# Performance work log

Measured on AMD Instinct MI355X. Metric: run time of the kernel, lower is better.

Reference implementation:

```python
import jax, jax.numpy as jnp
import numpy as np

WH, WW = 7, 7          # window size
SH, SW = 3, 3          # shift size
NUM_HEADS = 8


def setup_inputs() -> dict:
    key = jax.random.key(0)
    ks = jax.random.split(key, 5)
    B, H, W, C = 32, 56, 56, 256
    return {
        "x": jax.random.normal(ks[0], (B, H * W, C), dtype=jnp.float32),
        "w_qkv": jax.random.normal(ks[1], (C, 3 * C), dtype=jnp.float32) * (C ** -0.5),
        "b_qkv": jax.random.normal(ks[2], (3 * C,), dtype=jnp.float32) * 0.02,
        "w_proj": jax.random.normal(ks[3], (C, C), dtype=jnp.float32) * (C ** -0.5),
        "b_proj": jax.random.normal(ks[4], (C,), dtype=jnp.float32) * 0.02,
        "H": H,
        "W": W,
    }


def reference(x, w_qkv, b_qkv, w_proj, b_proj, H, W):
    B, N, C = x.shape
    nh = NUM_HEADS
    hd = C // nh
    nwh, nww = H // WH, W // WW

    xi = x.reshape(B, H, W, C)
    if SH > 0 or SW > 0:
        xi = jnp.roll(xi, shift=(-SH, -SW), axis=(1, 2))
    # window partition: [B*nwh*nww, WH*WW, C]
    xw = xi.reshape(B, nwh, WH, nww, WW, C).transpose(0, 1, 3, 2, 4, 5)
    xw = xw.reshape(-1, WH * WW, C)

    qkv = xw @ w_qkv + b_qkv                     # [nW, 49, 3C]
    qkv = qkv.reshape(-1, WH * WW, 3, nh, hd).transpose(2, 0, 3, 1, 4)
    q, k, v = qkv[0], qkv[1], qkv[2]             # each [nW, nh, 49, hd]

    attn = jnp.einsum('whqd,whkd->whqk', q, k) * (hd ** -0.5)
    attn = jax.nn.softmax(attn, axis=-1)
    out = jnp.einsum('whqk,whkd->whqd', attn, v)  # [nW, nh, 49, hd]
    out = out.transpose(0, 2, 1, 3).reshape(-1, WH * WW, C)
    out = out @ w_proj + b_proj

    # window merge
    out = out.reshape(B, nwh, nww, WH, WW, C).transpose(0, 1, 3, 2, 4, 5)
    out = out.reshape(B, H, W, C)
    if SH > 0 or SW > 0:
        out = jnp.roll(out, shift=(SH, SW), axis=(1, 2))
    return out.reshape(B, N, C)
```

## Files before the change

### kernel.cpp

```cpp
#include <hip/hip_runtime.h>
#include <hip/hip_bf16.h>

typedef __attribute__((ext_vector_type(4))) short bf16x4;
typedef __attribute__((ext_vector_type(8))) short bf16x8;
typedef __attribute__((ext_vector_type(4))) float f32x4;

#define MFMA32(A,B,C) __builtin_amdgcn_mfma_f32_16x16x32_bf16(A,B,C,0,0,0)
#define ROWB 528
#define ROWS 49

__device__ __forceinline__ short f2bf(float f) {
    __hip_bfloat16 h = __float2bfloat16(f);
    union { __hip_bfloat16 h; short s; } u; u.h = h;
    return u.s;
}

__global__ void prep_weights(const float* __restrict__ wqkv,
                             const float* __restrict__ wproj,
                             short* __restrict__ wqkvT,
                             short* __restrict__ wprojT) {
    const int n = blockIdx.x, k = threadIdx.x;
    if (n < 768) wqkvT[n * 256 + k] = f2bf(wqkv[k * 768 + n]);
    else         wprojT[(n - 768) * 256 + k] = f2bf(wproj[k * 256 + (n - 768)]);
}

__launch_bounds__(256, 2)
__global__ void winattn_fused(const float* __restrict__ x,
                              const float* __restrict__ bqkv,
                              const float* __restrict__ bproj,
                              const short* __restrict__ wqkvT,
                              const short* __restrict__ wprojT,
                              float* __restrict__ out) {
    __shared__ char smem[2 * ROWS * ROWB];
    char* cbuf = smem + ROWS * ROWB;
    const int tid = threadIdx.x;
    const int wid = blockIdx.x;
    const int b  = wid >> 6;
    const int wh = (wid >> 3) & 7;
    const int ww = wid & 7;

    {
        const int r   = tid >> 2;
        const int qtr = tid & 3;
        if (r < ROWS) {
            char* dst = smem + r * ROWB + qtr * 128;
            const int i = r / 7, j = r - i * 7;
            int h  = wh * 7 + i + 3; if (h  >= 56) h  -= 56;
            int wc = ww * 7 + j + 3; if (wc >= 56) wc -= 56;
            const float* src = x + (((size_t)(b * 56 + h)) * 56 + wc) * 256 + qtr * 64;
            #pragma unroll
            for (int c = 0; c < 8; ++c) {
                f32x4 f0 = *(const f32x4*)(src + c * 8);
                f32x4 f1 = *(const f32x4*)(src + c * 8 + 4);
                bf16x8 o;
                #pragma unroll
                for (int q = 0; q < 4; ++q) { o[q] = f2bf(f0[q]); o[q + 4] = f2bf(f1[q]); }
                *(bf16x8*)(dst + c * 16) = o;
            }
        }
    }
    __syncthreads();

    const int wv4 = tid >> 6;
    const int l   = tid & 63;
    const int l15 = l & 15;
    const int l4  = l >> 4;

    const char* xb[4];
    #pragma unroll
    for (int t = 0; t < 4; ++t) {
        int row = t * 16 + l15; if (row > 48) row = 48;
        xb[t] = smem + row * ROWB + (l4 << 4);
    }
    const int rowoff = l15 * 256 + (l4 << 3);

    #pragma unroll
    for (int hh = 0; hh < 2; ++hh) {
        const int head = (hh << 2) + wv4;
        const short* wqB = wqkvT + ((head << 5) << 8);
        const short* wkB = wqB + (256 << 8);
        const short* wvB = wqB + (512 << 8);

        bf16x8 qp[4], kp[4], vp[2][2];

        #pragma unroll
        for (int h = 0; h < 2; ++h) {
            f32x4 acc[4];
            #pragma unroll
            for (int t = 0; t < 4; ++t) acc[t] = (f32x4){0.f, 0.f, 0.f, 0.f};
            const short* wp = wqB + (h << 12) + rowoff;
            #pragma unroll
            for (int kk = 0; kk < 8; ++kk) {
                bf16x8 wf = *(const bf16x8*)(wp + (kk << 5));
                #pragma unroll
                for (int t = 0; t < 4; ++t) {
                    bf16x8 xf = *(const bf16x8*)(xb[t] + kk * 64);
                    acc[t] = MFMA32(wf, xf, acc[t]);
                }
            }
            f32x4 bq = *(const f32x4*)(bqkv + (head << 5) + h * 16 + (l4 << 2));
            #pragma unroll
            for (int t = 0; t < 4; ++t)
                #pragma unroll
                for (int rg = 0; rg < 4; ++rg)
                    qp[t][h * 4 + rg] = f2bf((acc[t][rg] + bq[rg]) * 0.17677669529663687f);
        }
        #pragma unroll
        for (int h = 0; h < 2; ++h) {
            f32x4 acc[4];
            #pragma unroll
            for (int t = 0; t < 4; ++t) acc[t] = (f32x4){0.f, 0.f, 0.f, 0.f};
            const short* wp = wkB + (h << 12) + rowoff;
            #pragma unroll
            for (int kk = 0; kk < 8; ++kk) {
                bf16x8 wf = *(const bf16x8*)(wp + (kk << 5));
                #pragma unroll
                for (int t = 0; t < 4; ++t) {
                    bf16x8 xf = *(const bf16x8*)(xb[t] + kk * 64);
                    acc[t] = MFMA32(wf, xf, acc[t]);
                }
            }
            f32x4 bk = *(const f32x4*)(bqkv + 256 + (head << 5) + h * 16 + (l4 << 2));
            #pragma unroll
            for (int t = 0; t < 4; ++t)
                #pragma unroll
                for (int rg = 0; rg < 4; ++rg)
                    kp[t][h * 4 + rg] = f2bf(acc[t][rg] + bk[rg]);
        }
        #pragma unroll
        for (int h = 0; h < 2; ++h) {
            f32x4 acc[4];
            #pragma unroll
            for (int t = 0; t < 4; ++t) acc[t] = (f32x4){0.f, 0.f, 0.f, 0.f};
            const short* wp = wvB + (h << 12) + rowoff;
            #pragma unroll
            for (int kk = 0; kk < 8; ++kk) {
                bf16x8 wf = *(const bf16x8*)(wp + (kk << 5));
                #pragma unroll
                for (int t = 0; t < 4; ++t) {
                    bf16x8 xf = *(const bf16x8*)(xb[t] + kk * 64);
                    acc[t] = MFMA32(xf, wf, acc[t]);
                }
            }
            const float bv = bqkv[512 + (head << 5) + h * 16 + l15];
            #pragma unroll
            for (int t = 0; t < 4; ++t)
                #pragma unroll
                for (int rg = 0; rg < 4; ++rg)
                    vp[t >> 1][h][(t & 1) * 4 + rg] = f2bf(acc[t][rg] + bv);
        }

        #pragma unroll
        for (int qt = 0; qt < 4; ++qt) {
            f32x4 sQ[4];
            #pragma unroll
            for (int t = 0; t < 4; ++t) sQ[t] = (f32x4){0.f, 0.f, 0.f, 0.f};
            #pragma unroll
            for (int t = 0; t < 4; ++t)
                sQ[t] = MFMA32(kp[t], qp[qt], sQ[t]);

            float m = -1e30f;
            #pragma unroll
            for (int t = 0; t < 4; ++t)
                #pragma unroll
                for (int rg = 0; rg < 4; ++rg) {
                    const bool valid = (t < 3) || ((l4 | rg) == 0);
                    float v0 = valid ? sQ[t][rg] : -1e30f;
                    sQ[t][rg] = v0;
                    m = fmaxf(m, v0);
                }
            m = fmaxf(m, __shfl_xor(m, 16));
            m = fmaxf(m, __shfl_xor(m, 32));
            float s = 0.f;
            #pragma unroll
            for (int t = 0; t < 4; ++t)
                #pragma unroll
                for (int rg = 0; rg < 4; ++rg) {
                    float e = __expf(sQ[t][rg] - m);
                    sQ[t][rg] = e;
                    s += e;
                }
            s += __shfl_xor(s, 16);
            s += __shfl_xor(s, 32);
            const float inv = 1.f / s;

            bf16x8 pf[2];
            #pragma unroll
            for (int t = 0; t < 4; ++t)
                #pragma unroll
                for (int rg = 0; rg < 4; ++rg)
                    pf[t >> 1][(t & 1) * 4 + rg] = f2bf(sQ[t][rg] * inv);

            const int row = qt * 16 + l15;
            #pragma unroll
            for (int h = 0; h < 2; ++h) {
                f32x4 oq = (f32x4){0.f, 0.f, 0.f, 0.f};
                oq = MFMA32(vp[0][h], pf[0], oq);
                oq = MFMA32(vp[1][h], pf[1], oq);
                if (row < ROWS) {
                    bf16x4 ob;
                    #pragma unroll
                    for (int rg = 0; rg < 4; ++rg) ob[rg] = f2bf(oq[rg]);
                    const int colbyte = ((head << 5) + (h << 4) + (l4 << 2)) * 2;
                    *(bf16x4*)(cbuf + row * ROWB + colbyte) = ob;
                }
            }
        }
    }
    __syncthreads();

    const char* ab[4];
    #pragma unroll
    for (int rt = 0; rt < 4; ++rt) {
        int row = rt * 16 + l15; if (row > 48) row = 48;
        ab[rt] = cbuf + row * ROWB + (l4 << 4);
    }
    const int hb = wh * 7 + 3;
    const int wb = ww * 7 + 3;

    #pragma unroll
    for (int g = 0; g < 2; ++g) {
        const int colbase = (wv4 << 6) + (g << 5);
        f32x4 po[2][4];
        #pragma unroll
        for (int c = 0; c < 2; ++c)
            #pragma unroll
            for (int r = 0; r < 4; ++r) po[c][r] = (f32x4){0.f, 0.f, 0.f, 0.f};

        const short* pb[2];
        #pragma unroll
        for (int ct = 0; ct < 2; ++ct)
            pb[ct] = wprojT + ((colbase + (ct << 4) + l15) << 8) + (l4 << 3);

        #pragma unroll
        for (int kk = 0; kk < 8; ++kk) {
            bf16x8 a[4];
            #pragma unroll
            for (int rt = 0; rt < 4; ++rt) a[rt] = *(const bf16x8*)(ab[rt] + kk * 64);
            #pragma unroll
            for (int ct = 0; ct < 2; ++ct) {
                bf16x8 bfr = *(const bf16x8*)(pb[ct] + (kk << 5));
                #pragma unroll
                for (int rt = 0; rt < 4; ++rt)
                    po[ct][rt] = MFMA32(a[rt], bfr, po[ct][rt]);
            }
        }

        #pragma unroll
        for (int ct = 0; ct < 2; ++ct) {
            const int col = colbase + (ct << 4) + l15;
            const float bias = bproj[col];
            #pragma unroll
            for (int rt = 0; rt < 4; ++rt) {
                const int r0 = rt * 16 + (l4 << 2);
                int i = r0 / 7;
                int j = r0 - i * 7;
                #pragma unroll
                for (int rg = 0; rg < 4; ++rg) {
                    const int row = r0 + rg;
                    if (row < 49) {
                        int h  = hb + i; if (h  >= 56) h  -= 56;
                        int wc = wb + j; if (wc >= 56) wc -= 56;
                        out[(((size_t)(b * 56 + h)) * 56 + wc) * 256 + col] = po[ct][rt][rg] + bias;
                    }
                    ++j; if (j == 7) { j = 0; ++i; }
                }
            }
        }
    }
}

extern "C" void kernel_launch(void* const* d_in, const int* in_sizes, int n_in,
                              void* d_out, int out_size, void* d_ws, size_t ws_size,
                              hipStream_t stream) {
    const float* x     = (const float*)d_in[0];
    const float* wqkv  = (const float*)d_in[1];
    const float* bqkv  = (const float*)d_in[2];
    const float* wproj = (const float*)d_in[3];
    const float* bproj = (const float*)d_in[4];
    float* out = (float*)d_out;

    short* wqkvT  = (short*)d_ws;
    short* wprojT = wqkvT + 768 * 256;

    prep_weights<<<dim3(1024), dim3(256), 0, stream>>>(wqkv, wproj, wqkvT, wprojT);
    winattn_fused<<<dim3(2048), dim3(256), 0, stream>>>(x, bqkv, bproj, wqkvT, wprojT, out);
}
```

Baseline: 153.1 us.

## Reuse single LDS buffer for attention output by staging head-0 result in registers

Shrinks shared memory from two 49-row buffers to one. The first head's attention output is held in registers until both heads' QKV projections have read x from LDS. After a barrier, the context output overwrites the x buffer. The softmax normalization also moves after the PV matmul, scaling the 16 outputs per row instead of the probabilities. Halving LDS per block could allow more resident blocks, at the cost of extra registers for the staged outputs, which may push register pressure against the 2-block launch bound.

After: 176.9 us. 1.16x slower.

```diff
diff --git a/kernel.cpp b/kernel.cpp
--- a/kernel.cpp
+++ b/kernel.cpp
@@ -24,6 +24,114 @@
     else         wprojT[(n - 768) * 256 + k] = f2bf(wproj[k * 256 + (n - 768)]);
 }
 
+__device__ __forceinline__ void qkv_pass(const short* __restrict__ wqB,
+                                         const float* __restrict__ bqkv, int head,
+                                         const char* const xb[4],
+                                         int rowoff, int l4, int l15,
+                                         bf16x8 qp[4], bf16x8 kp[4], bf16x8 vp[2][2]) {
+    #pragma unroll
+    for (int h = 0; h < 2; ++h) {
+        f32x4 acc[4];
+        #pragma unroll
+        for (int t = 0; t < 4; ++t) acc[t] = (f32x4){0.f, 0.f, 0.f, 0.f};
+        const short* wp = wqB + (h << 12) + rowoff;
+        #pragma unroll
+        for (int kk = 0; kk < 8; ++kk) {
+            bf16x8 wf = *(const bf16x8*)(wp + (kk << 5));
+            #pragma unroll
+            for (int t = 0; t < 4; ++t) {
+                bf16x8 xf = *(const bf16x8*)(xb[t] + kk * 64);
+                acc[t] = MFMA32(wf, xf, acc[t]);
+            }
+        }
+        f32x4 bq = *(const f32x4*)(bqkv + (head << 5) + h * 16 + (l4 << 2));
+        #pragma unroll
+        for (int t = 0; t < 4; ++t)
+            #pragma unroll
+            for (int rg = 0; rg < 4; ++rg)
+                qp[t][h * 4 + rg] = f2bf((acc[t][rg] + bq[rg]) * 0.17677669529663687f);
+    }
+    #pragma unroll
+    for (int h = 0; h < 2; ++h) {
+        f32x4 acc[4];
+        #pragma unroll
+        for (int t = 0; t < 4; ++t) acc[t] = (f32x4){0.f, 0.f, 0.f, 0.f};
+        const short* wp = wqB + (256 << 8) + (h << 12) + rowoff;
+        #pragma unroll
+        for (int kk = 0; kk < 8; ++kk) {
+            bf16x8 wf = *(const bf16x8*)(wp + (kk << 5));
+            #pragma unroll
+            for (int t = 0; t < 4; ++t) {
+                bf16x8 xf = *(const bf16x8*)(xb[t] + kk * 64);
+                acc[t] = MFMA32(wf, xf, acc[t]);
+            }
+        }
+        f32x4 bk = *(const f32x4*)(bqkv + 256 + (head << 5) + h * 16 + (l4 << 2));
+        #pragma unroll
+        for (int t = 0; t < 4; ++t)
+            #pragma unroll
+            for (int rg = 0; rg < 4; ++rg)
+                kp[t][h * 4 + rg] = f2bf(acc[t][rg] + bk[rg]);
+    }
+    #pragma unroll
+    for (int h = 0; h < 2; ++h) {
+        f32x4 acc[4];
+        #pragma unroll
+        for (int t = 0; t < 4; ++t) acc[t] = (f32x4){0.f, 0.f, 0.f, 0.f};
+        const short* wp = wqB + (512 << 8) + (h << 12) + rowoff;
+        #pragma unroll
+        for (int kk = 0; kk < 8; ++kk) {
+            bf16x8 wf = *(const bf16x8*)(wp + (kk << 5));
+            #pragma unroll
+            for (int t = 0; t < 4; ++t) {
+                bf16x8 xf = *(const bf16x8*)(xb[t] + kk * 64);
+                acc[t] = MFMA32(xf, wf, acc[t]);
+            }
+        }
+        const float bv = bqkv[512 + (head << 5) + h * 16 + l15];
+        #pragma unroll
+        for (int t = 0; t < 4; ++t)
+            #pragma unroll
+            for (int rg = 0; rg < 4; ++rg)
+                vp[t >> 1][h][(t & 1) * 4 + rg] = f2bf(acc[t][rg] + bv);
+    }
+}
+
+__device__ __forceinline__ float attn_pf(const bf16x8 kp[4], bf16x8 qpqt, int l4,
+                                         bf16x8 pf[2]) {
+    f32x4 sQ[4];
+    #pragma unroll
+    for (int t = 0; t < 4; ++t) sQ[t] = (f32x4){0.f, 0.f, 0.f, 0.f};
+    #pragma unroll
+    for (int t = 0; t < 4; ++t)
+        sQ[t] = MFMA32(kp[t], qpqt, sQ[t]);
+
+    float m = -1e30f;
+    #pragma unroll
+    for (int t = 0; t < 4; ++t)
+        #pragma unroll
+        for (int rg = 0; rg < 4; ++rg) {
+            const bool valid = (t < 3) || ((l4 | rg) == 0);
+            float v0 = valid ? sQ[t][rg] : -1e30f;
+            sQ[t][rg] = v0;
+            m = fmaxf(m, v0);
+        }
+    m = fmaxf(m, __shfl_xor(m, 16));
+    m = fmaxf(m, __shfl_xor(m, 32));
+    float s = 0.f;
+    #pragma unroll
+    for (int t = 0; t < 4; ++t)
+        #pragma unroll
+        for (int rg = 0; rg < 4; ++rg) {
+            float e = __expf(sQ[t][rg] - m);
+            pf[t >> 1][(t & 1) * 4 + rg] = f2bf(e);
+            s += e;
+        }
+    s += __shfl_xor(s, 16);
+    s += __shfl_xor(s, 32);
+    return 1.f / s;
+}
+
 __launch_bounds__(256, 2)
 __global__ void winattn_fused(const float* __restrict__ x,
                               const float* __restrict__ bqkv,
@@ -31,8 +139,7 @@
                               const short* __restrict__ wqkvT,
                               const short* __restrict__ wprojT,
                               float* __restrict__ out) {
-    __shared__ char smem[2 * ROWS * ROWB];
-    char* cbuf = smem + ROWS * ROWB;
+    __shared__ char smem[ROWS * ROWB];
     const int tid = threadIdx.x;
     const int wid = blockIdx.x;
     const int b  = wid >> 6;
@@ -74,136 +181,59 @@
     }
     const int rowoff = l15 * 256 + (l4 << 3);
 
-    #pragma unroll
-    for (int hh = 0; hh < 2; ++hh) {
-        const int head = (hh << 2) + wv4;
-        const short* wqB = wqkvT + ((head << 5) << 8);
-        const short* wkB = wqB + (256 << 8);
-        const short* wvB = wqB + (512 << 8);
-
-        bf16x8 qp[4], kp[4], vp[2][2];
-
-        #pragma unroll
-        for (int h = 0; h < 2; ++h) {
-            f32x4 acc[4];
-            #pragma unroll
-            for (int t = 0; t < 4; ++t) acc[t] = (f32x4){0.f, 0.f, 0.f, 0.f};
-            const short* wp = wqB + (h << 12) + rowoff;
-            #pragma unroll
-            for (int kk = 0; kk < 8; ++kk) {
-                bf16x8 wf = *(const bf16x8*)(wp + (kk << 5));
-                #pragma unroll
-                for (int t = 0; t < 4; ++t) {
-                    bf16x8 xf = *(const bf16x8*)(xb[t] + kk * 64);
-                    acc[t] = MFMA32(wf, xf, acc[t]);
-                }
-            }
-            f32x4 bq = *(const f32x4*)(bqkv + (head << 5) + h * 16 + (l4 << 2));
-            #pragma unroll
-            for (int t = 0; t < 4; ++t)
-                #pragma unroll
-                for (int rg = 0; rg < 4; ++rg)
-                    qp[t][h * 4 + rg] = f2bf((acc[t][rg] + bq[rg]) * 0.17677669529663687f);
-        }
-        #pragma unroll
-        for (int h = 0; h < 2; ++h) {
-            f32x4 acc[4];
-            #pragma unroll
-            for (int t = 0; t < 4; ++t) acc[t] = (f32x4){0.f, 0.f, 0.f, 0.f};
-            const short* wp = wkB + (h << 12) + rowoff;
-            #pragma unroll
-            for (int kk = 0; kk < 8; ++kk) {
-                bf16x8 wf = *(const bf16x8*)(wp + (kk << 5));
-                #pragma unroll
-                for (int t = 0; t < 4; ++t) {
-                    bf16x8 xf = *(const bf16x8*)(xb[t] + kk * 64);
-                    acc[t] = MFMA32(wf, xf, acc[t]);
-                }
-            }
-            f32x4 bk = *(const f32x4*)(bqkv + 256 + (head << 5) + h * 16 + (l4 << 2));
-            #pragma unroll
-            for (int t = 0; t < 4; ++t)
-                #pragma unroll
-                for (int rg = 0; rg < 4; ++rg)
-                    kp[t][h * 4 + rg] = f2bf(acc[t][rg] + bk[rg]);
-        }
-        #pragma unroll
-        for (int h = 0; h < 2; ++h) {
-            f32x4 acc[4];
-            #pragma unroll
-            for (int t = 0; t < 4; ++t) acc[t] = (f32x4){0.f, 0.f, 0.f, 0.f};
-            const short* wp = wvB + (h << 12) + rowoff;
-            #pragma unroll
-            for (int kk = 0; kk < 8; ++kk) {
-                bf16x8 wf = *(const bf16x8*)(wp + (kk << 5));
-                #pragma unroll
-                for (int t = 0; t < 4; ++t) {
-                    bf16x8 xf = *(const bf16x8*)(xb[t] + kk * 64);
-                    acc[t] = MFMA32(xf, wf, acc[t]);
-                }
-            }
-            const float bv = bqkv[512 + (head << 5) + h * 16 + l15];
-            #pragma unroll
-            for (int t = 0; t < 4; ++t)
-                #pragma unroll
-                for (int rg = 0; rg < 4; ++rg)
-                    vp[t >> 1][h][(t & 1) * 4 + rg] = f2bf(acc[t][rg] + bv);
-        }
-
+    bf16x8 qp[4], kp[4], vp[2][2];
+    bf16x4 oreg0[4][2];
+
+    {
+        const int head = wv4;
+        qkv_pass(wqkvT + ((head << 5) << 8), bqkv, head, xb, rowoff, l4, l15, qp, kp, vp);
         #pragma unroll
         for (int qt = 0; qt < 4; ++qt) {
-            f32x4 sQ[4];
-            #pragma unroll
-            for (int t = 0; t < 4; ++t) sQ[t] = (f32x4){0.f, 0.f, 0.f, 0.f};
-            #pragma unroll
-            for (int t = 0; t < 4; ++t)
-                sQ[t] = MFMA32(kp[t], qp[qt], sQ[t]);
-
-            float m = -1e30f;
-            #pragma unroll
-            for (int t = 0; t < 4; ++t)
-                #pragma unroll
-                for (int rg = 0; rg < 4; ++rg) {
-                    const bool valid = (t < 3) || ((l4 | rg) == 0);
-                    float v0 = valid ? sQ[t][rg] : -1e30f;
-                    sQ[t][rg] = v0;
-                    m = fmaxf(m, v0);
-                }
-            m = fmaxf(m, __shfl_xor(m, 16));
-            m = fmaxf(m, __shfl_xor(m, 32));
-            float s = 0.f;
-            #pragma unroll
-            for (int t = 0; t < 4; ++t)
-                #pragma unroll
-                for (int rg = 0; rg < 4; ++rg) {
-                    float e = __expf(sQ[t][rg] - m);
-                    sQ[t][rg] = e;
-                    s += e;
-                }
-            s += __shfl_xor(s, 16);
-            s += __shfl_xor(s, 32);
-            const float inv = 1.f / s;
-
             bf16x8 pf[2];
-            #pragma unroll
-            for (int t = 0; t < 4; ++t)
-                #pragma unroll
-                for (int rg = 0; rg < 4; ++rg)
-                    pf[t >> 1][(t & 1) * 4 + rg] = f2bf(sQ[t][rg] * inv);
-
-            const int row = qt * 16 + l15;
+            const float inv = attn_pf(kp, qp[qt], l4, pf);
             #pragma unroll
             for (int h = 0; h < 2; ++h) {
                 f32x4 oq = (f32x4){0.f, 0.f, 0.f, 0.f};
                 oq = MFMA32(vp[0][h], pf[0], oq);
                 oq = MFMA32(vp[1][h], pf[1], oq);
-                if (row < ROWS) {
-                    bf16x4 ob;
-                    #pragma unroll
-                    for (int rg = 0; rg < 4; ++rg) ob[rg] = f2bf(oq[rg]);
-                    const int colbyte = ((head << 5) + (h << 4) + (l4 << 2)) * 2;
-                    *(bf16x4*)(cbuf + row * ROWB + colbyte) = ob;
-                }
+                #pragma unroll
+                for (int rg = 0; rg < 4; ++rg) oreg0[qt][h][rg] = f2bf(oq[rg] * inv);
+            }
+        }
+    }
+
+    const int head1 = 4 + wv4;
+    qkv_pass(wqkvT + ((head1 << 5) << 8), bqkv, head1, xb, rowoff, l4, l15, qp, kp, vp);
+    __syncthreads();
+
+    {
+        const int head = wv4;
+        #pragma unroll
+        for (int qt = 0; qt < 4; ++qt) {
+            const int row = qt * 16 + l15;
+            if (row < ROWS) {
+                const int colbyte = ((head << 5) + (l4 << 2)) * 2;
+                *(bf16x4*)(smem + row * ROWB + colbyte)      = oreg0[qt][0];
+                *(bf16x4*)(smem + row * ROWB + colbyte + 32) = oreg0[qt][1];
+            }
+        }
+    }
+    #pragma unroll
+    for (int qt = 0; qt < 4; ++qt) {
+        bf16x8 pf[2];
+        const float inv = attn_pf(kp, qp[qt], l4, pf);
+        const int row = qt * 16 + l15;
+        #pragma unroll
+        for (int h = 0; h < 2; ++h) {
+            f32x4 oq = (f32x4){0.f, 0.f, 0.f, 0.f};
+            oq = MFMA32(vp[0][h], pf[0], oq);
+            oq = MFMA32(vp[1][h], pf[1], oq);
+            if (row < ROWS) {
+                bf16x4 ob;
+                #pragma unroll
+                for (int rg = 0; rg < 4; ++rg) ob[rg] = f2bf(oq[rg] * inv);
+                const int colbyte = ((head1 << 5) + (h << 4) + (l4 << 2)) * 2;
+                *(bf16x4*)(smem + row * ROWB + colbyte) = ob;
             }
         }
     }
@@ -213,7 +243,7 @@
     #pragma unroll
     for (int rt = 0; rt < 4; ++rt) {
         int row = rt * 16 + l15; if (row > 48) row = 48;
-        ab[rt] = cbuf + row * ROWB + (l4 << 4);
+        ab[rt] = smem + row * ROWB + (l4 << 4);
     }
     const int hb = wh * 7 + 3;
     const int wb = ww * 7 + 3;
```
